# Optimization experiments

Measured on AMD Instinct MI355X. Metric: run time of the kernel, lower is better.

## Reference

```python
import jax, jax.numpy as jnp
import numpy as np

B = 131072
D_IN = 128
D_H = 128


def _linear_params(key, fan_in, fan_out):
    # mimic nn.Linear init: U(-1/sqrt(fan_in), 1/sqrt(fan_in))
    kw, kb = jax.random.split(key)
    bound = 1.0 / np.sqrt(fan_in)
    W = jax.random.uniform(kw, (fan_in, fan_out), minval=-bound, maxval=bound, dtype=jnp.float32)
    b = jax.random.uniform(kb, (fan_out,), minval=-bound, maxval=bound, dtype=jnp.float32)
    return W, b


def setup_inputs() -> dict:
    key = jax.random.key(0)
    ks = jax.random.split(key, 12)
    inp = {
        'input': jax.random.normal(ks[0], (B, D_IN), dtype=jnp.float32),
        'seq_input': jax.random.normal(ks[1], (B, D_IN), dtype=jnp.float32),
        'hidden': jax.random.normal(ks[2], (B, D_H), dtype=jnp.float32),
    }
    names = ['ir', 'iz', 'in_', 'sr', 'sz', 'sn', 'hr', 'hz', 'hn']
    for i, nm in enumerate(names):
        fan_in = D_H if nm.startswith('h') else D_IN
        W, b = _linear_params(ks[3 + i], fan_in, D_H)
        inp['W_' + nm] = W
        inp['b_' + nm] = b
    return inp


def reference(input, seq_input, hidden,
              W_ir, b_ir, W_iz, b_iz, W_in_, b_in_,
              W_sr, b_sr, W_sz, b_sz, W_sn, b_sn,
              W_hr, b_hr, W_hz, b_hz, W_hn, b_hn):
    def lin(x, W, b):
        return x @ W + b

    hr = lin(hidden, W_hr, b_hr)  # shared between r_input and r_seq
    r_input = jax.nn.sigmoid(lin(input, W_ir, b_ir) + hr)
    r_seq = jax.nn.sigmoid(lin(seq_input, W_sr, b_sr) + hr)
    r = (r_input + r_seq) * 0.5

    hz = lin(hidden, W_hz, b_hz)
    z_input = jax.nn.sigmoid(lin(input, W_iz, b_iz) + hz)
    z_seq = jax.nn.sigmoid(lin(seq_input, W_sz, b_sz) + hz)
    z = (z_input + z_seq) * 0.5

    n = jnp.tanh(lin(input, W_in_, b_in_) + lin(seq_input, W_sn, b_sn)
                 + lin(r * hidden, W_hn, b_hn))
    new_hidden = (1.0 - z) * n + z * hidden
    return new_hidden
```

## Files before the change

kernel.cpp:

```cpp
#include <hip/hip_runtime.h>

#define BDIM 512
#define PACK_BDIM 256

typedef __attribute__((ext_vector_type(8))) short bf16x8;
typedef __attribute__((ext_vector_type(4))) float f32x4;
typedef __attribute__((ext_vector_type(4))) unsigned int u32x4;

__device__ __forceinline__ unsigned short f2b(float x) {
    unsigned u = __float_as_uint(x);
    return (unsigned short)((u + 0x7fffu + ((u >> 16) & 1u)) >> 16);
}
__device__ __forceinline__ float b2f(unsigned short b) {
    return __uint_as_float(((unsigned)b) << 16);
}

typedef __attribute__((address_space(1))) const unsigned int ga_u32;
typedef __attribute__((address_space(3))) unsigned int la_u32;
__device__ __forceinline__ void gload_lds16(const void* g, void* l) {
    __builtin_amdgcn_global_load_lds((ga_u32*)g, (la_u32*)l, 16, 0, 0);
}

__global__ __launch_bounds__(PACK_BDIM) void pack_weights(
    const float* __restrict__ w0, const float* __restrict__ w1,
    const float* __restrict__ w2, const float* __restrict__ w3,
    const float* __restrict__ w4, const float* __restrict__ w5,
    const float* __restrict__ w6, const float* __restrict__ w7,
    const float* __restrict__ w8, unsigned short* __restrict__ wp)
{
    __shared__ float wsm[16384];
    const float* W;
    switch (blockIdx.x) {
        case 0: W = w0; break; case 1: W = w1; break; case 2: W = w2; break;
        case 3: W = w3; break; case 4: W = w4; break; case 5: W = w5; break;
        case 6: W = w6; break; case 7: W = w7; break; default: W = w8; break;
    }
    const int tid = threadIdx.x;
    for (int i = tid; i < 16384; i += PACK_BDIM) wsm[i] = W[i];
    __syncthreads();
    unsigned short* dst = wp + (size_t)blockIdx.x * 32768;
    for (int item = tid; item < 4096; item += PACK_BDIM) {
        const int lane = item & 63, q = item >> 6;
        const int s = q >> 5, cf = q & 31, c = cf >> 3, f = cf & 7;
        const int k0 = c * 32 + (lane >> 4) * 8;
        const int n  = f * 16 + (lane & 15);
        unsigned v2[4];
        for (int i2 = 0; i2 < 4; i2++) {
            unsigned short lohi[2];
            for (int t = 0; t < 2; t++) {
                float x = wsm[(k0 + i2 * 2 + t) * 128 + n];
                unsigned short hb = f2b(x);
                if (s) { hb = (unsigned short)(__float_as_uint(x - b2f(hb)) >> 16); }
                lohi[t] = hb;
            }
            v2[i2] = (unsigned)lohi[0] | ((unsigned)lohi[1] << 16);
        }
        u32x4 vv; vv[0] = v2[0]; vv[1] = v2[1]; vv[2] = v2[2]; vv[3] = v2[3];
        *(u32x4*)(dst + (size_t)(s * 32 + cf) * 512 + lane * 8) = vv;
    }
}

__global__ __launch_bounds__(BDIM, 2) void gru_fused(
    const float* __restrict__ inp, const float* __restrict__ seqp,
    const float* __restrict__ hid, const unsigned short* __restrict__ wp,
    const float* __restrict__ b_ir, const float* __restrict__ b_iz,
    const float* __restrict__ b_in, const float* __restrict__ b_sr,
    const float* __restrict__ b_sz, const float* __restrict__ b_sn,
    const float* __restrict__ b_hr, const float* __restrict__ b_hz,
    const float* __restrict__ b_hn, float* __restrict__ outp)
{
    __shared__ unsigned short whbuf[16384];
    __shared__ __align__(16) float rbuf[64 * 132];

    const int tid    = threadIdx.x;
    const int lane   = tid & 63;
    const int wid    = tid >> 6;
    const int rowgrp = wid >> 1;
    const int colgrp = wid & 1;
    const int agrp   = lane >> 4;
    const int a16    = lane & 15;
    const int ncol0  = colgrp * 64;
    const size_t row0 = (size_t)blockIdx.x * 64;
    const int locrow_a = rowgrp * 16 + a16;

    const float* pAin  = inp  + (row0 + locrow_a) * 128;
    const float* pAseq = seqp + (row0 + locrow_a) * 128;
    const float* pAhid = hid  + (row0 + locrow_a) * 128;

    f32x4 hx[4], t[4], s1[4], nacc[4];
    const f32x4 zv = {0.f, 0.f, 0.f, 0.f};

    auto stage = [&](int g, int s) {
        const char* src = (const char*)wp + (size_t)g * 65536 + (size_t)s * 32768;
        #pragma unroll
        for (int j = 0; j < 4; j++) {
            const int off = (j * 8 + wid) * 1024;
            gload_lds16(src + off + lane * 16, (char*)whbuf + off);
        }
    };

    auto phase = [&](int g, f32x4* acc, const float* pA, bool withR, bool init) {
        __syncthreads();
        stage(g, 0);
        bf16x8 ah[4], al[4];
        #pragma unroll
        for (int c = 0; c < 4; c++) {
            const float* p = pA + c * 32 + agrp * 8;
            f32x4 x0 = *(const f32x4*)(p);
            f32x4 x1 = *(const f32x4*)(p + 4);
            if (withR) {
                const int rk = c * 32 + agrp * 8;
                x0 *= *(const f32x4*)(&rbuf[locrow_a * 132 + rk]);
                x1 *= *(const f32x4*)(&rbuf[locrow_a * 132 + rk + 4]);
            }
            #pragma unroll
            for (int i = 0; i < 4; i++) {
                unsigned short hb = f2b(x0[i]);
                ah[c][i] = (short)hb;
                al[c][i] = (short)(__float_as_uint(x0[i] - b2f(hb)) >> 16);
                unsigned short hb1 = f2b(x1[i]);
                ah[c][4 + i] = (short)hb1;
                al[c][4 + i] = (short)(__float_as_uint(x1[i] - b2f(hb1)) >> 16);
            }
        }
        if (init) {
            #pragma unroll
            for (int f = 0; f < 4; f++) acc[f] = zv;
        }
        __syncthreads();
        #pragma unroll
        for (int c = 0; c < 4; c++)
            #pragma unroll
            for (int f = 0; f < 4; f++) {
                const int fglob = colgrp * 4 + f;
                const bf16x8 wh = *(const bf16x8*)(&whbuf[(size_t)(c * 8 + fglob) * 512 + lane * 8]);
                acc[f] = __builtin_amdgcn_mfma_f32_16x16x32_bf16(ah[c], wh, acc[f], 0, 0, 0);
                acc[f] = __builtin_amdgcn_mfma_f32_16x16x32_bf16(al[c], wh, acc[f], 0, 0, 0);
            }
        __syncthreads();
        stage(g, 1);
        __syncthreads();
        #pragma unroll
        for (int c = 0; c < 4; c++)
            #pragma unroll
            for (int f = 0; f < 4; f++) {
                const int fglob = colgrp * 4 + f;
                const bf16x8 wl = *(const bf16x8*)(&whbuf[(size_t)(c * 8 + fglob) * 512 + lane * 8]);
                acc[f] = __builtin_amdgcn_mfma_f32_16x16x32_bf16(ah[c], wl, acc[f], 0, 0, 0);
            }
    };

    auto addb = [&](f32x4* acc, const float* b) {
        #pragma unroll
        for (int f = 0; f < 4; f++) {
            float bv = b[ncol0 + f * 16 + a16];
            #pragma unroll
            for (int j = 0; j < 4; j++) acc[f][j] += bv;
        }
    };

    auto sigm = [](float x) { return 1.f / (1.f + __expf(-x)); };
    auto tanh_ = [](float x) {
        x = fminf(18.f, fmaxf(-18.f, x));
        float e = __expf(2.f * x);
        return (e - 1.f) / (e + 1.f);
    };

    phase(6, hx, pAhid, false, true); addb(hx, b_hr);
    phase(0, t, pAin, false, true);  addb(t, b_ir);
    #pragma unroll
    for (int f = 0; f < 4; f++)
        #pragma unroll
        for (int j = 0; j < 4; j++) s1[f][j] = sigm(t[f][j] + hx[f][j]);
    phase(3, t, pAseq, false, true); addb(t, b_sr);
    #pragma unroll
    for (int f = 0; f < 4; f++)
        #pragma unroll
        for (int j = 0; j < 4; j++) {
            int row = rowgrp * 16 + agrp * 4 + j;
            int col = ncol0 + f * 16 + a16;
            rbuf[row * 132 + col] = 0.5f * (s1[f][j] + sigm(t[f][j] + hx[f][j]));
        }

    phase(2, nacc, pAin, false, true);  addb(nacc, b_in);
    phase(5, nacc, pAseq, false, false); addb(nacc, b_sn);
    phase(8, nacc, pAhid, true, false);  addb(nacc, b_hn);

    phase(7, hx, pAhid, false, true); addb(hx, b_hz);
    phase(1, t, pAin, false, true);  addb(t, b_iz);
    #pragma unroll
    for (int f = 0; f < 4; f++)
        #pragma unroll
        for (int j = 0; j < 4; j++) s1[f][j] = sigm(t[f][j] + hx[f][j]);
    phase(4, t, pAseq, false, true); addb(t, b_sz);

    #pragma unroll
    for (int f = 0; f < 4; f++)
        #pragma unroll
        for (int j = 0; j < 4; j++) {
            int row = rowgrp * 16 + agrp * 4 + j;
            int col = ncol0 + f * 16 + a16;
            float zz = 0.5f * (s1[f][j] + sigm(t[f][j] + hx[f][j]));
            float h  = hid[(row0 + row) * 128 + col];
            float nn = tanh_(nacc[f][j]);
            rbuf[row * 132 + col] = (1.f - zz) * nn + zz * h;
        }
    __syncthreads();
    #pragma unroll
    for (int p = 0; p < 4; p++) {
        int e = p * 2048 + tid * 4;
        int rrow = e >> 7, c0 = e & 127;
        f32x4 v = *(const f32x4*)(&rbuf[rrow * 132 + c0]);
        *(f32x4*)(&outp[(row0 + rrow) * 128 + c0]) = v;
    }
}

extern "C" void kernel_launch(void* const* d_in, const int* in_sizes, int n_in,
                              void* d_out, int out_size, void* d_ws, size_t ws_size,
                              hipStream_t stream)
{
    (void)in_sizes; (void)n_in; (void)out_size; (void)ws_size;
    const float* inp  = (const float*)d_in[0];
    const float* seqp = (const float*)d_in[1];
    const float* hid  = (const float*)d_in[2];
    const float* W[9]; const float* Bv[9];
    for (int i = 0; i < 9; i++) {
        W[i]  = (const float*)d_in[3 + 2 * i];
        Bv[i] = (const float*)d_in[4 + 2 * i];
    }
    unsigned short* wp = (unsigned short*)d_ws;

    pack_weights<<<9, PACK_BDIM, 0, stream>>>(W[0], W[1], W[2], W[3], W[4],
                                              W[5], W[6], W[7], W[8], wp);
    gru_fused<<<2048, BDIM, 0, stream>>>(inp, seqp, hid, wp,
                                         Bv[0], Bv[1], Bv[2], Bv[3], Bv[4],
                                         Bv[5], Bv[6], Bv[7], Bv[8],
                                         (float*)d_out);
}
```

Baseline: 317.7 us.

## Alias r/output staging buffer onto weight LDS with XOR swizzle

```diff
diff --git a/kernel.cpp b/kernel.cpp
--- a/kernel.cpp
+++ b/kernel.cpp
@@ -69,8 +69,8 @@
     const float* __restrict__ b_hr, const float* __restrict__ b_hz,
     const float* __restrict__ b_hn, float* __restrict__ outp)
 {
-    __shared__ unsigned short whbuf[16384];
-    __shared__ __align__(16) float rbuf[64 * 132];
+    __shared__ __align__(16) unsigned short whbuf[16384];
+    float* tb = (float*)whbuf;
 
     const int tid    = threadIdx.x;
     const int lane   = tid & 63;
@@ -82,12 +82,13 @@
     const int ncol0  = colgrp * 64;
     const size_t row0 = (size_t)blockIdx.x * 64;
     const int locrow_a = rowgrp * 16 + a16;
+    const int rswA = (locrow_a & 7) << 3;
 
     const float* pAin  = inp  + (row0 + locrow_a) * 128;
     const float* pAseq = seqp + (row0 + locrow_a) * 128;
     const float* pAhid = hid  + (row0 + locrow_a) * 128;
 
-    f32x4 hx[4], t[4], s1[4], nacc[4];
+    f32x4 hx[4], t[4], s1[4], nacc[4], rA[8];
     const f32x4 zv = {0.f, 0.f, 0.f, 0.f};
 
     auto stage = [&](int g, int s) {
@@ -99,7 +100,7 @@
         }
     };
 
-    auto phase = [&](int g, f32x4* acc, const float* pA, bool withR, bool init) {
+    auto phase = [&](int g, f32x4* acc, const float* pA, const f32x4* rAv, bool init) {
         __syncthreads();
         stage(g, 0);
         bf16x8 ah[4], al[4];
@@ -108,11 +109,7 @@
             const float* p = pA + c * 32 + agrp * 8;
             f32x4 x0 = *(const f32x4*)(p);
             f32x4 x1 = *(const f32x4*)(p + 4);
-            if (withR) {
-                const int rk = c * 32 + agrp * 8;
-                x0 *= *(const f32x4*)(&rbuf[locrow_a * 132 + rk]);
-                x1 *= *(const f32x4*)(&rbuf[locrow_a * 132 + rk + 4]);
-            }
+            if (rAv) { x0 *= rAv[2 * c]; x1 *= rAv[2 * c + 1]; }
             #pragma unroll
             for (int i = 0; i < 4; i++) {
                 unsigned short hb = f2b(x0[i]);
@@ -166,34 +163,45 @@
         return (e - 1.f) / (e + 1.f);
     };
 
-    phase(6, hx, pAhid, false, true); addb(hx, b_hr);
-    phase(0, t, pAin, false, true);  addb(t, b_ir);
+    phase(6, hx, pAhid, nullptr, true); addb(hx, b_hr);
+    phase(0, t, pAin, nullptr, true);  addb(t, b_ir);
     #pragma unroll
     for (int f = 0; f < 4; f++)
         #pragma unroll
         for (int j = 0; j < 4; j++) s1[f][j] = sigm(t[f][j] + hx[f][j]);
-    phase(3, t, pAseq, false, true); addb(t, b_sr);
+    phase(3, t, pAseq, nullptr, true); addb(t, b_sr);
+
+    __syncthreads();
     #pragma unroll
     for (int f = 0; f < 4; f++)
         #pragma unroll
         for (int j = 0; j < 4; j++) {
             int row = rowgrp * 16 + agrp * 4 + j;
             int col = ncol0 + f * 16 + a16;
-            rbuf[row * 132 + col] = 0.5f * (s1[f][j] + sigm(t[f][j] + hx[f][j]));
-        }
-
-    phase(2, nacc, pAin, false, true);  addb(nacc, b_in);
-    phase(5, nacc, pAseq, false, false); addb(nacc, b_sn);
-    phase(8, nacc, pAhid, true, false);  addb(nacc, b_hn);
-
-    phase(7, hx, pAhid, false, true); addb(hx, b_hz);
-    phase(1, t, pAin, false, true);  addb(t, b_iz);
+            tb[row * 128 + (col ^ ((row & 7) << 3))] =
+                0.5f * (s1[f][j] + sigm(t[f][j] + hx[f][j]));
+        }
+    __syncthreads();
+    #pragma unroll
+    for (int c = 0; c < 4; c++) {
+        int rk = (c * 32 + agrp * 8) ^ rswA;
+        rA[2 * c]     = *(const f32x4*)(&tb[locrow_a * 128 + rk]);
+        rA[2 * c + 1] = *(const f32x4*)(&tb[locrow_a * 128 + rk + 4]);
+    }
+
+    phase(8, nacc, pAhid, rA, true);      addb(nacc, b_hn);
+    phase(2, nacc, pAin, nullptr, false);  addb(nacc, b_in);
+    phase(5, nacc, pAseq, nullptr, false); addb(nacc, b_sn);
+
+    phase(7, hx, pAhid, nullptr, true); addb(hx, b_hz);
+    phase(1, t, pAin, nullptr, true);  addb(t, b_iz);
     #pragma unroll
     for (int f = 0; f < 4; f++)
         #pragma unroll
         for (int j = 0; j < 4; j++) s1[f][j] = sigm(t[f][j] + hx[f][j]);
-    phase(4, t, pAseq, false, true); addb(t, b_sz);
-
+    phase(4, t, pAseq, nullptr, true); addb(t, b_sz);
+
+    __syncthreads();
     #pragma unroll
     for (int f = 0; f < 4; f++)
         #pragma unroll
@@ -203,14 +211,14 @@
             float zz = 0.5f * (s1[f][j] + sigm(t[f][j] + hx[f][j]));
             float h  = hid[(row0 + row) * 128 + col];
             float nn = tanh_(nacc[f][j]);
-            rbuf[row * 132 + col] = (1.f - zz) * nn + zz * h;
+            tb[row * 128 + (col ^ ((row & 7) << 3))] = (1.f - zz) * nn + zz * h;
         }
     __syncthreads();
     #pragma unroll
     for (int p = 0; p < 4; p++) {
         int e = p * 2048 + tid * 4;
         int rrow = e >> 7, c0 = e & 127;
-        f32x4 v = *(const f32x4*)(&rbuf[rrow * 132 + c0]);
+        f32x4 v = *(const f32x4*)(&tb[rrow * 128 + (c0 ^ ((rrow & 7) << 3))]);
         *(f32x4*)(&outp[(row0 + rrow) * 128 + c0]) = v;
     }
 }
```

Result: no change. 312.1 us (-1.8%).
